# Optimization experiments

Hardware: AMD Instinct MI355X
Metric: run time of the kernel (lower is better)

The kernel has to match this reference:

```python
import jax, jax.numpy as jnp
import numpy as np

B, N, D_IN, D_MEM = 32, 1024, 512, 512
LN_EPS = 1e-5


def setup_inputs() -> dict:
    key = jax.random.key(0)
    ks = jax.random.split(key, 6)
    adj = jax.random.uniform(ks[0], (B, N, N), dtype=jnp.float32)
    input_emb = jax.random.normal(ks[1], (B * N, D_IN), dtype=jnp.float32)
    seq_lens = jnp.full((B,), N, dtype=jnp.int64) if jax.config.jax_enable_x64 else jnp.full((B,), N, dtype=jnp.int32)
    scale = 1.0 / np.sqrt(D_IN)
    W0_w = jax.random.normal(ks[2], (D_MEM, D_IN), dtype=jnp.float32) * scale
    W0_b = jax.random.normal(ks[3], (D_MEM,), dtype=jnp.float32) * 0.01
    W1_w = jax.random.normal(ks[4], (D_MEM, D_MEM), dtype=jnp.float32) * scale
    W1_b = jax.random.normal(ks[5], (D_MEM,), dtype=jnp.float32) * 0.01
    ln_g = jnp.ones((D_MEM,), dtype=jnp.float32)
    ln_b = jnp.zeros((D_MEM,), dtype=jnp.float32)
    return {"adj": adj, "input_emb": input_emb, "seq_lens": seq_lens,
            "W0_w": W0_w, "W0_b": W0_b, "W1_w": W1_w, "W1_b": W1_b,
            "ln_g": ln_g, "ln_b": ln_b}


def _layer_norm(x, g, b):
    mu = jnp.mean(x, axis=-1, keepdims=True)
    var = jnp.mean(jnp.square(x - mu), axis=-1, keepdims=True)
    return (x - mu) * jax.lax.rsqrt(var + LN_EPS) * g + b


def reference(adj, input_emb, seq_lens, W0_w, W0_b, W1_w, W1_b, ln_g, ln_b):
    # All seq_lens == N, so pad_sequence(split(input_emb)) is a pure reshape.
    x = input_emb.reshape(B, N, D_IN)  # dropout probs are 0 -> identity
    denom = jnp.sum(adj, axis=2, keepdims=True) + 1.0           # [B,N,1]
    masks = ((jnp.sum(adj, axis=2) + jnp.sum(adj, axis=1)) == 0)[..., None]  # [B,N,1]
    for Ww, Wb in ((W0_w, W0_b), (W1_w, W1_b)):
        Ax = jnp.einsum('bnm,bmd->bnd', adj, x)                 # adj.bmm(x)
        # W(Ax) + W(x) == (Ax + x) @ W^T + 2b
        AxW = (Ax + x) @ Ww.T + 2.0 * Wb
        x = jax.nn.relu(AxW / denom)                            # gcn_drop p=0
    out = _layer_norm(x, ln_g, ln_b)                            # norm_flag=True
    return out, masks
```

## Files before the change

### kernel.cpp

```cpp
#include <hip/hip_runtime.h>
#include <stdint.h>

typedef __bf16 bf16_t;
typedef __bf16 bf16x8 __attribute__((ext_vector_type(8)));
typedef float  f32x4  __attribute__((ext_vector_type(4)));

#define GLD_LDS(gp, lp) __builtin_amdgcn_global_load_lds( \
    (const __attribute__((address_space(1))) void*)(gp),  \
    (__attribute__((address_space(3))) void*)(lp), 16, 0, 0)

__global__ void probe_kernel(const unsigned int* __restrict__ w, int* __restrict__ flag)
{
    const int lane = threadIdx.x;
    bool ok = true;
#pragma unroll
    for (int i = 0; i < 4; ++i) {
        unsigned x = w[lane * 4 + i];
        unsigned lo = x & 0xffffu, hi = x >> 16;
        ok = ok && (lo <= 0x3F80u) && (hi <= 0x3F80u);
    }
    unsigned long long m = __ballot(ok);
    if (lane == 0) *flag = (m == ~0ULL) ? 1 : 0;
}

__device__ __forceinline__ void gemm_mainloop(const bf16_t* __restrict__ Ag,
                                              const bf16_t* __restrict__ Bg,
                                              int K, bf16_t* Abuf, bf16_t* Bbuf,
                                              f32x4 acc[4][4])
{
    const int t    = threadIdx.x;
    const int wave = t >> 6;
    const int lane = t & 63;
    const int srow = (wave << 5) + (lane >> 3);
    const int sc   = ((lane & 7) ^ (lane >> 3)) << 3;
    const bf16_t* aP = Ag + (size_t)srow * K + sc;
    const bf16_t* bP = Bg + (size_t)srow * K + sc;
    const size_t rskip = (size_t)8 * K;
    bf16_t* aL = Abuf + (wave << 11);
    bf16_t* bL = Bbuf + (wave << 11);
    const int wm   = (wave & 1) << 6;
    const int wn   = (wave >> 1) << 6;
    const int lrow = lane & 15;
    const int quad = lane >> 4;
    const int g    = lrow & 7;
    const int so[2] = { (quad ^ g) << 3, ((4 | quad) ^ g) << 3 };

#pragma unroll
    for (int i = 0; i < 4; ++i)
#pragma unroll
        for (int j = 0; j < 4; ++j)
#pragma unroll
            for (int r = 0; r < 4; ++r) acc[i][j][r] = 0.0f;

    for (int kk = 0; kk < K; kk += 64) {
#pragma unroll
        for (int p = 0; p < 4; ++p) {
            GLD_LDS(aP + p * rskip, aL + (p << 9));
            GLD_LDS(bP + p * rskip, bL + (p << 9));
        }
        aP += 64; bP += 64;
        __syncthreads();

#pragma unroll
        for (int s = 0; s < 2; ++s) {
            bf16x8 af[4], bfv[4];
#pragma unroll
            for (int i = 0; i < 4; ++i) {
                af[i]  = *(const bf16x8*)(Abuf + ((wm + (i << 4) + lrow) << 6) + so[s]);
                bfv[i] = *(const bf16x8*)(Bbuf + ((wn + (i << 4) + lrow) << 6) + so[s]);
            }
#pragma unroll
            for (int i = 0; i < 4; ++i)
#pragma unroll
                for (int j = 0; j < 4; ++j)
                    acc[i][j] = __builtin_amdgcn_mfma_f32_16x16x32_bf16(af[i], bfv[j], acc[i][j], 0, 0, 0);
        }
        __syncthreads();
    }
}

__global__ __launch_bounds__(256) void bmm_kernel(const void* __restrict__ adj_in,
                                                  const bf16_t* __restrict__ adj_ws,
                                                  const bf16_t* __restrict__ xT,
                                                  const void* __restrict__ xadd,
                                                  int xadd_bf16,
                                                  const int* __restrict__ flag,
                                                  bf16_t* __restrict__ zout)
{
    __shared__ __align__(16) bf16_t Abuf[8192];
    __shared__ __align__(16) bf16_t Bbuf[8192];
    const int is_bf = *flag;
    const bf16_t* adj = is_bf ? (const bf16_t*)adj_in : adj_ws;
    const int id   = blockIdx.x;
    const int xcd  = id & 7;
    const int slot = id >> 3;
    const int n0   = (slot & 3) << 7;
    const int m0   = ((slot >> 2) & 7) << 7;
    const int b    = (xcd << 2) | (slot >> 5);
    const bf16_t* Ag = adj + (size_t)b * 1048576 + (size_t)m0 * 1024;
    const bf16_t* Bg = xT  + (size_t)b * 524288  + (size_t)n0 * 1024;
    f32x4 acc[4][4];
    gemm_mainloop(Ag, Bg, 1024, Abuf, Bbuf, acc);

    const int lane = threadIdx.x & 63;
    const int wave = threadIdx.x >> 6;
    const int wm = (wave & 1) << 6, wn = (wave >> 1) << 6;
    const int lrow = lane & 15, quad = lane >> 4;
    const int xf32 = (!xadd_bf16) && (!is_bf);
    const size_t rowbase = (size_t)b * 1024 + m0;
#pragma unroll
    for (int i = 0; i < 4; ++i)
#pragma unroll
        for (int j = 0; j < 4; ++j)
#pragma unroll
            for (int r = 0; r < 4; ++r) {
                int row = wm + (i << 4) + (quad << 2) + r;
                int col = n0 + wn + (j << 4) + lrow;
                size_t idx = (rowbase + row) * 512 + col;
                float xa = xf32 ? ((const float*)xadd)[idx]
                                : (float)((const bf16_t*)xadd)[idx];
                zout[idx] = (bf16_t)(acc[i][j][r] + xa);
            }
}

__global__ __launch_bounds__(256) void wgemm_kernel(const bf16_t* __restrict__ z,
                                                    const bf16_t* __restrict__ W,
                                                    const float* __restrict__ bias,
                                                    const float* __restrict__ rowsum,
                                                    bf16_t* __restrict__ out)
{
    __shared__ __align__(16) bf16_t Abuf[8192];
    __shared__ __align__(16) bf16_t Bbuf[8192];
    const int m0 = blockIdx.x * 128;
    const int n0 = blockIdx.y * 128;
    const bf16_t* Ag = z + (size_t)m0 * 512;
    const bf16_t* Bg = W + (size_t)n0 * 512;
    f32x4 acc[4][4];
    gemm_mainloop(Ag, Bg, 512, Abuf, Bbuf, acc);

    const int lane = threadIdx.x & 63;
    const int wave = threadIdx.x >> 6;
    const int wm = (wave & 1) << 6, wn = (wave >> 1) << 6;
    const int lrow = lane & 15, quad = lane >> 4;
    float bi[4];
#pragma unroll
    for (int j = 0; j < 4; ++j) bi[j] = 2.0f * bias[n0 + wn + (j << 4) + lrow];
#pragma unroll
    for (int i = 0; i < 4; ++i)
#pragma unroll
        for (int r = 0; r < 4; ++r) {
            int row = m0 + wm + (i << 4) + (quad << 2) + r;
            float inv_dn = 1.0f / (rowsum[row] + 1.0f);
#pragma unroll
            for (int j = 0; j < 4; ++j) {
                int col = n0 + wn + (j << 4) + lrow;
                float v = fmaxf((acc[i][j][r] + bi[j]) * inv_dn, 0.0f);
                out[(size_t)row * 512 + col] = (bf16_t)v;
            }
        }
}

__global__ __launch_bounds__(256) void transpose_kernel(const void* __restrict__ in,
                                                        bf16_t* __restrict__ out,
                                                        const int* __restrict__ flag,
                                                        int force_bf16)
{
    __shared__ float tile[64][65];
    const int f32 = (!force_bf16) && (*flag == 0);
    const int b  = blockIdx.z;
    const int n0 = blockIdx.x * 64;
    const int d0 = blockIdx.y * 64;
    const int t  = threadIdx.x;
    const size_t base = ((size_t)b * 1024 + n0) * 512 + d0;
#pragma unroll
    for (int pass = 0; pass < 2; ++pass) {
        int r = pass * 32 + (t >> 3);
        int c = (t & 7) << 3;
        size_t off = base + (size_t)r * 512 + c;
        if (f32) {
            const float4* p = (const float4*)((const float*)in + off);
            float4 a = p[0], q = p[1];
            tile[r][c+0]=a.x; tile[r][c+1]=a.y; tile[r][c+2]=a.z; tile[r][c+3]=a.w;
            tile[r][c+4]=q.x; tile[r][c+5]=q.y; tile[r][c+6]=q.z; tile[r][c+7]=q.w;
        } else {
            bf16x8 v = *(const bf16x8*)((const bf16_t*)in + off);
#pragma unroll
            for (int k = 0; k < 8; ++k) tile[r][c + k] = (float)v[k];
        }
    }
    __syncthreads();
    bf16_t* dst = out + ((size_t)b * 512 + d0) * 1024 + n0;
#pragma unroll
    for (int pass = 0; pass < 2; ++pass) {
        int d = pass * 32 + (t >> 3);
        int c = (t & 7) << 3;
        bf16x8 v;
#pragma unroll
        for (int k = 0; k < 8; ++k) v[k] = (bf16_t)tile[c + k][d];
        *(bf16x8*)(dst + (size_t)d * 1024 + c) = v;
    }
}

__global__ __launch_bounds__(256) void adjrow_kernel(const void* __restrict__ adj,
                                                     const int* __restrict__ flag,
                                                     bf16_t* __restrict__ adj_b,
                                                     float* __restrict__ rowsum)
{
    const int row  = blockIdx.x * 4 + (threadIdx.x >> 6);
    const int lane = threadIdx.x & 63;
    const int f32  = (*flag == 0);
    const size_t base = (size_t)row * 1024 + lane * 16;
    float v[16];
    if (f32) {
        const float4* p = (const float4*)((const float*)adj + base);
#pragma unroll
        for (int i = 0; i < 4; ++i) {
            float4 q = p[i];
            v[i*4+0]=q.x; v[i*4+1]=q.y; v[i*4+2]=q.z; v[i*4+3]=q.w;
        }
    } else {
        const bf16x8* p = (const bf16x8*)((const bf16_t*)adj + base);
        bf16x8 q0 = p[0], q1 = p[1];
#pragma unroll
        for (int k = 0; k < 8; ++k) { v[k] = (float)q0[k]; v[8+k] = (float)q1[k]; }
    }
    float s = 0.0f;
#pragma unroll
    for (int k = 0; k < 16; ++k) s += v[k];
    if (f32) {
        bf16x8 o0, o1;
#pragma unroll
        for (int k = 0; k < 8; ++k) { o0[k] = (bf16_t)v[k]; o1[k] = (bf16_t)v[8+k]; }
        *(bf16x8*)(adj_b + base)     = o0;
        *(bf16x8*)(adj_b + base + 8) = o1;
    }
#pragma unroll
    for (int off = 32; off > 0; off >>= 1) s += __shfl_down(s, off);
    if (lane == 0) rowsum[row] = s;
}

__global__ __launch_bounds__(256) void colsum_kernel(const void* __restrict__ adj_in,
                                                     const bf16_t* __restrict__ adj_ws,
                                                     const int* __restrict__ flag,
                                                     float* __restrict__ colsum)
{
    const bf16_t* a = (*flag) ? (const bf16_t*)adj_in : adj_ws;
    const int b = blockIdx.y;
    const int c = blockIdx.x * 256 + threadIdx.x;
    const int r0 = blockIdx.z * 256;
    const bf16_t* p = a + (size_t)b * 1048576 + (size_t)r0 * 1024 + c;
    float s = 0.0f;
#pragma unroll 8
    for (int r = 0; r < 256; ++r) s += (float)p[(size_t)r * 1024];
    atomicAdd(&colsum[b * 1024 + c], s);
}

__global__ __launch_bounds__(256) void mask_kernel(const float* __restrict__ rowsum,
                                                   const float* __restrict__ colsum,
                                                   void* __restrict__ out,
                                                   const int* __restrict__ flag)
{
    const int i = blockIdx.x * 256 + threadIdx.x;
    float m = (rowsum[i] + colsum[i] == 0.0f) ? 1.0f : 0.0f;
    if (*flag) ((bf16_t*)out)[16777216 + i] = (bf16_t)m;
    else       ((float*)out)[16777216 + i]  = m;
}

__global__ __launch_bounds__(256) void canon_small(const void* __restrict__ W0,
                                                   const void* __restrict__ W1,
                                                   const void* __restrict__ b0,
                                                   const void* __restrict__ b1,
                                                   const void* __restrict__ g,
                                                   const void* __restrict__ bt,
                                                   const int* __restrict__ flag,
                                                   bf16_t* __restrict__ W0ws,
                                                   bf16_t* __restrict__ W1ws,
                                                   float* __restrict__ par,
                                                   float* __restrict__ colsum)
{
    const int idx = blockIdx.x * 256 + threadIdx.x;
    const int f32 = (*flag == 0);
#define RD(p, i) (f32 ? ((const float*)(p))[i] : (float)((const bf16_t*)(p))[i])
    if      (idx < 262144) W0ws[idx]          = (bf16_t)RD(W0, idx);
    else if (idx < 524288) W1ws[idx - 262144] = (bf16_t)RD(W1, idx - 262144);
    else if (idx < 524800) par[idx - 524288]  = RD(b0, idx - 524288);
    else if (idx < 525312) par[idx - 524288]  = RD(b1, idx - 524800);
    else if (idx < 525824) par[idx - 524288]  = RD(g,  idx - 525312);
    else if (idx < 526336) par[idx - 524288]  = RD(bt, idx - 525824);
    else if (idx < 559104) colsum[idx - 526336] = 0.0f;
#undef RD
}

__global__ __launch_bounds__(256) void ln_kernel(const bf16_t* __restrict__ x,
                                                 const float* __restrict__ g,
                                                 const float* __restrict__ bb,
                                                 void* __restrict__ out,
                                                 const int* __restrict__ flag)
{
    const int row  = blockIdx.x * 4 + (threadIdx.x >> 6);
    const int lane = threadIdx.x & 63;
    bf16x8 xv = *(const bf16x8*)(x + (size_t)row * 512 + lane * 8);
    float vv[8], s = 0.0f, ss = 0.0f;
#pragma unroll
    for (int k = 0; k < 8; ++k) { vv[k] = (float)xv[k]; s += vv[k]; ss += vv[k] * vv[k]; }
#pragma unroll
    for (int off = 32; off > 0; off >>= 1) { s += __shfl_down(s, off); ss += __shfl_down(ss, off); }
    s = __shfl(s, 0); ss = __shfl(ss, 0);
    const float mu   = s * (1.0f / 512.0f);
    const float var  = ss * (1.0f / 512.0f) - mu * mu;
    const float rstd = rsqrtf(var + 1e-5f);
    float o[8];
#pragma unroll
    for (int k = 0; k < 8; ++k)
        o[k] = (vv[k] - mu) * rstd * g[lane * 8 + k] + bb[lane * 8 + k];
    const size_t obase = (size_t)row * 512 + lane * 8;
    if (*flag) {
        bf16x8 ob;
#pragma unroll
        for (int k = 0; k < 8; ++k) ob[k] = (bf16_t)o[k];
        *(bf16x8*)((bf16_t*)out + obase) = ob;
    } else {
        float4 o0 = {o[0], o[1], o[2], o[3]}, o1 = {o[4], o[5], o[6], o[7]};
        *(float4*)((float*)out + obase)     = o0;
        *(float4*)((float*)out + obase + 4) = o1;
    }
}

extern "C" void kernel_launch(void* const* d_in, const int* in_sizes, int n_in,
                              void* d_out, int out_size, void* d_ws, size_t ws_size,
                              hipStream_t stream)
{
    const void* adj  = d_in[0];
    const void* x0   = d_in[1];
    const void* W0w  = d_in[3];
    const void* W0b  = d_in[4];
    const void* W1w  = d_in[5];
    const void* W1b  = d_in[6];
    const void* lng  = d_in[7];
    const void* lnb  = d_in[8];

    char* ws = (char*)d_ws;
    bf16_t* adj_ws = (bf16_t*)ws;
    bf16_t* x2     = (bf16_t*)ws;
    bf16_t* z_buf  = (bf16_t*)(ws + 67108864);
    bf16_t* x1     = (bf16_t*)(ws + 100663296);
    bf16_t* W0ws   = (bf16_t*)(ws + 134217728);
    bf16_t* W1ws   = (bf16_t*)(ws + 134742016);
    float*  par    = (float*)(ws + 135266304);
    float*  rowsum = (float*)(ws + 135274496);
    float*  colsum = (float*)(ws + 135405568);
    int*    flag   = (int*)(ws + 135536640);

    bf16_t* xT = (bf16_t*)d_out;

    probe_kernel<<<1, 64, 0, stream>>>((const unsigned int*)adj, flag);
    canon_small<<<2184, 256, 0, stream>>>(W0w, W1w, W0b, W1b, lng, lnb, flag,
                                          W0ws, W1ws, par, colsum);
    adjrow_kernel<<<8192, 256, 0, stream>>>(adj, flag, adj_ws, rowsum);
    colsum_kernel<<<dim3(4, 32, 4), 256, 0, stream>>>(adj, adj_ws, flag, colsum);
    mask_kernel<<<128, 256, 0, stream>>>(rowsum, colsum, d_out, flag);

    transpose_kernel<<<dim3(16, 8, 32), 256, 0, stream>>>(x0, xT, flag, 0);
    bmm_kernel<<<1024, 256, 0, stream>>>(adj, adj_ws, xT, x0, 0, flag, z_buf);
    wgemm_kernel<<<dim3(256, 4), 256, 0, stream>>>(z_buf, W0ws, par, rowsum, x1);

    transpose_kernel<<<dim3(16, 8, 32), 256, 0, stream>>>(x1, xT, flag, 1);
    bmm_kernel<<<1024, 256, 0, stream>>>(adj, adj_ws, xT, x1, 1, flag, z_buf);
    wgemm_kernel<<<dim3(256, 4), 256, 0, stream>>>(z_buf, W1ws, par + 512, rowsum, x2);

    ln_kernel<<<8192, 256, 0, stream>>>(x2, par + 1024, par + 1536, d_out, flag);
}
```

Measured before the change: 522.2 us.

## Rewrite GEMM mainloop as 256x256 tile with double-buffered 8-wave ping-pong pipeline

Replaces the 128x128 single-buffered GEMM mainloop, used by both the batched adjacency matmul and the weight GEMM, with a 256x256 tile on 512 threads. The new loop double-buffers A and B in 128KB of dynamic LDS and interleaves direct global-to-LDS loads with MFMA phases, using barriers, priority hints and vmcnt waits. The goal is to hide memory latency behind compute and double operand reuse per tile. In exchange the grids shrink to 256 blocks, which may under-fill the GPU, and register pressure rises with 32 accumulators per lane.

```diff
diff --git a/kernel.cpp b/kernel.cpp
--- a/kernel.cpp
+++ b/kernel.cpp
@@ -23,137 +23,192 @@
     if (lane == 0) *flag = (m == ~0ULL) ? 1 : 0;
 }
 
-__device__ __forceinline__ void gemm_mainloop(const bf16_t* __restrict__ Ag,
-                                              const bf16_t* __restrict__ Bg,
-                                              int K, bf16_t* Abuf, bf16_t* Bbuf,
-                                              f32x4 acc[4][4])
+#define STAGE_HALF(dstE, gp) do { \
+    GLD_LDS((gp) + (size_t)r0 * K + cS,        lds + (dstE) + t * 8); \
+    GLD_LDS((gp) + (size_t)(r0 + 64) * K + cS, lds + (dstE) + 4096 + t * 8); } while (0)
+
+#define STG_A(d, h, k0) STAGE_HALF((d)*16384 + (h)*8192, Ag + (size_t)(h)*128*K + (k0))
+#define STG_B(d, h, k0) STAGE_HALF(32768 + (d)*16384 + (h)*8192, Bg + (size_t)(h)*128*K + (k0))
+
+#define LDA(af, d, mq) do { _Pragma("unroll") for (int i_ = 0; i_ < 4; ++i_) { \
+    const bf16_t* p_ = lds + (d)*16384 + aBase + (((mq)*64) + (i_ << 4) + lrow) * 64; \
+    af[i_][0] = *(const bf16x8*)(p_ + so0); \
+    af[i_][1] = *(const bf16x8*)(p_ + so1); } } while (0)
+
+#define LDB(bfv, d, nq) do { _Pragma("unroll") for (int j_ = 0; j_ < 2; ++j_) { \
+    const bf16_t* p_ = lds + bBase + (d)*16384 + (((nq)*32) + (j_ << 4) + lrow) * 64; \
+    bfv[j_][0] = *(const bf16x8*)(p_ + so0); \
+    bfv[j_][1] = *(const bf16x8*)(p_ + so1); } } while (0)
+
+#define MFMA_Q(af, bfv, mq, nq) do { _Pragma("unroll") for (int i_ = 0; i_ < 4; ++i_) \
+    _Pragma("unroll") for (int j_ = 0; j_ < 2; ++j_) { \
+    acc[(mq)*4+i_][(nq)*2+j_] = __builtin_amdgcn_mfma_f32_16x16x32_bf16(af[i_][0], bfv[j_][0], acc[(mq)*4+i_][(nq)*2+j_], 0, 0, 0); \
+    acc[(mq)*4+i_][(nq)*2+j_] = __builtin_amdgcn_mfma_f32_16x16x32_bf16(af[i_][1], bfv[j_][1], acc[(mq)*4+i_][(nq)*2+j_], 0, 0, 0); } } while (0)
+
+#define PHASE_SYNC() do { __builtin_amdgcn_s_barrier(); \
+    asm volatile("s_waitcnt lgkmcnt(0)" ::: "memory"); \
+    __builtin_amdgcn_sched_barrier(0); \
+    __builtin_amdgcn_s_setprio(1); } while (0)
+
+#define PHASE_END() do { __builtin_amdgcn_s_setprio(0); \
+    __builtin_amdgcn_s_barrier(); } while (0)
+
+#define PHASE_END_VM() do { __builtin_amdgcn_s_setprio(0); \
+    asm volatile("s_waitcnt vmcnt(4)" ::: "memory"); \
+    __builtin_amdgcn_s_barrier(); } while (0)
+
+__device__ __forceinline__ void gemm256_mainloop(const bf16_t* __restrict__ Ag,
+                                                 const bf16_t* __restrict__ Bg,
+                                                 const int K, bf16_t* lds,
+                                                 f32x4 acc[8][4])
 {
     const int t    = threadIdx.x;
     const int wave = t >> 6;
     const int lane = t & 63;
-    const int srow = (wave << 5) + (lane >> 3);
-    const int sc   = ((lane & 7) ^ (lane >> 3)) << 3;
-    const bf16_t* aP = Ag + (size_t)srow * K + sc;
-    const bf16_t* bP = Bg + (size_t)srow * K + sc;
-    const size_t rskip = (size_t)8 * K;
-    bf16_t* aL = Abuf + (wave << 11);
-    bf16_t* bL = Bbuf + (wave << 11);
-    const int wm   = (wave & 1) << 6;
-    const int wn   = (wave >> 1) << 6;
+    const int wr   = wave >> 2;
+    const int wc   = wave & 3;
     const int lrow = lane & 15;
     const int quad = lane >> 4;
     const int g    = lrow & 7;
-    const int so[2] = { (quad ^ g) << 3, ((4 | quad) ^ g) << 3 };
-
-#pragma unroll
-    for (int i = 0; i < 4; ++i)
+
+    const int r0 = t >> 3;
+    const int cS = ((t & 7) ^ ((t >> 3) & 7)) << 3;
+
+    const int aBase = wr * 8192;
+    const int bBase = 32768 + ((wc >> 1) * 8192) + ((wc & 1) * 4096);
+    const int so0 = (quad ^ g) << 3;
+    const int so1 = ((4 | quad) ^ g) << 3;
+
+#pragma unroll
+    for (int i = 0; i < 8; ++i)
 #pragma unroll
         for (int j = 0; j < 4; ++j)
 #pragma unroll
             for (int r = 0; r < 4; ++r) acc[i][j][r] = 0.0f;
 
-    for (int kk = 0; kk < K; kk += 64) {
-#pragma unroll
-        for (int p = 0; p < 4; ++p) {
-            GLD_LDS(aP + p * rskip, aL + (p << 9));
-            GLD_LDS(bP + p * rskip, bL + (p << 9));
-        }
-        aP += 64; bP += 64;
-        __syncthreads();
-
-#pragma unroll
-        for (int s = 0; s < 2; ++s) {
-            bf16x8 af[4], bfv[4];
-#pragma unroll
-            for (int i = 0; i < 4; ++i) {
-                af[i]  = *(const bf16x8*)(Abuf + ((wm + (i << 4) + lrow) << 6) + so[s]);
-                bfv[i] = *(const bf16x8*)(Bbuf + ((wn + (i << 4) + lrow) << 6) + so[s]);
-            }
-#pragma unroll
-            for (int i = 0; i < 4; ++i)
-#pragma unroll
-                for (int j = 0; j < 4; ++j)
-                    acc[i][j] = __builtin_amdgcn_mfma_f32_16x16x32_bf16(af[i], bfv[j], acc[i][j], 0, 0, 0);
-        }
-        __syncthreads();
-    }
-}
-
-__global__ __launch_bounds__(256) void bmm_kernel(const void* __restrict__ adj_in,
-                                                  const bf16_t* __restrict__ adj_ws,
-                                                  const bf16_t* __restrict__ xT,
-                                                  const void* __restrict__ xadd,
-                                                  int xadd_bf16,
-                                                  const int* __restrict__ flag,
-                                                  bf16_t* __restrict__ zout)
-{
-    __shared__ __align__(16) bf16_t Abuf[8192];
-    __shared__ __align__(16) bf16_t Bbuf[8192];
+    STG_A(0, 0, 0); STG_A(0, 1, 0);
+    STG_B(0, 0, 0); STG_B(0, 1, 0);
+    STG_B(1, 0, 64); STG_B(1, 1, 64);
+    asm volatile("s_waitcnt vmcnt(4)" ::: "memory");
+    __builtin_amdgcn_s_barrier();
+
+    const int NT  = K >> 6;
+    const int NIT = NT >> 1;
+
+    bf16x8 af0[4][2], af1[4][2], ba[2][2], bb[2][2];
+
+    for (int it = 0; it < NIT; ++it) {
+        const int kA1 = (2 * it + 1) << 6;
+        const int k2  = ((2 * it + 2) < NT ? (2 * it + 2) : 0) << 6;
+        const int k3  = ((2 * it + 3) < NT ? (2 * it + 3) : 0) << 6;
+
+        LDA(af0, 0, 0); LDB(ba, 0, 0); STG_A(1, 0, kA1);
+        PHASE_SYNC(); MFMA_Q(af0, ba, 0, 0); PHASE_END();
+
+        LDB(bb, 0, 1); STG_A(1, 1, kA1);
+        PHASE_SYNC(); MFMA_Q(af0, bb, 0, 1); PHASE_END();
+
+        LDA(af1, 0, 1); STG_B(0, 0, k2);
+        PHASE_SYNC(); MFMA_Q(af1, ba, 1, 0); PHASE_END();
+
+        STG_B(0, 1, k2);
+        PHASE_SYNC(); MFMA_Q(af1, bb, 1, 1); PHASE_END_VM();
+
+        LDA(af0, 1, 0); LDB(ba, 1, 0); STG_A(0, 0, k2);
+        PHASE_SYNC(); MFMA_Q(af0, ba, 0, 0); PHASE_END();
+
+        LDB(bb, 1, 1); STG_A(0, 1, k2);
+        PHASE_SYNC(); MFMA_Q(af0, bb, 0, 1); PHASE_END();
+
+        LDA(af1, 1, 1); STG_B(1, 0, k3);
+        PHASE_SYNC(); MFMA_Q(af1, ba, 1, 0); PHASE_END();
+
+        STG_B(1, 1, k3);
+        PHASE_SYNC(); MFMA_Q(af1, bb, 1, 1); PHASE_END_VM();
+    }
+    asm volatile("s_waitcnt vmcnt(0)" ::: "memory");
+}
+
+__global__ __launch_bounds__(512, 2) void bmm_kernel(const void* __restrict__ adj_in,
+                                                     const bf16_t* __restrict__ adj_ws,
+                                                     const bf16_t* __restrict__ xT,
+                                                     const void* __restrict__ xadd,
+                                                     int xadd_bf16,
+                                                     const int* __restrict__ flag,
+                                                     bf16_t* __restrict__ zout)
+{
+    extern __shared__ __align__(16) bf16_t lds[];
     const int is_bf = *flag;
     const bf16_t* adj = is_bf ? (const bf16_t*)adj_in : adj_ws;
     const int id   = blockIdx.x;
     const int xcd  = id & 7;
-    const int slot = id >> 3;
-    const int n0   = (slot & 3) << 7;
-    const int m0   = ((slot >> 2) & 7) << 7;
-    const int b    = (xcd << 2) | (slot >> 5);
-    const bf16_t* Ag = adj + (size_t)b * 1048576 + (size_t)m0 * 1024;
-    const bf16_t* Bg = xT  + (size_t)b * 524288  + (size_t)n0 * 1024;
-    f32x4 acc[4][4];
-    gemm_mainloop(Ag, Bg, 1024, Abuf, Bbuf, acc);
+    const int s    = id >> 3;
+    const int b    = (xcd << 2) | (s >> 3);
+    const int tl   = s & 7;
+    const int mt   = tl >> 1;
+    const int nt2  = tl & 1;
+    const bf16_t* Ag = adj + (size_t)b * 1048576 + (size_t)mt * 262144;
+    const bf16_t* Bg = xT  + (size_t)b * 524288  + (size_t)nt2 * 262144;
+    f32x4 acc[8][4];
+    gemm256_mainloop(Ag, Bg, 1024, lds, acc);
 
     const int lane = threadIdx.x & 63;
     const int wave = threadIdx.x >> 6;
-    const int wm = (wave & 1) << 6, wn = (wave >> 1) << 6;
+    const int wr = wave >> 2, wc = wave & 3;
     const int lrow = lane & 15, quad = lane >> 4;
     const int xf32 = (!xadd_bf16) && (!is_bf);
-    const size_t rowbase = (size_t)b * 1024 + m0;
-#pragma unroll
-    for (int i = 0; i < 4; ++i)
+    const size_t rowbase = (size_t)b * 1024 + mt * 256 + wr * 128;
+    const int colbase = nt2 * 256 + wc * 64;
+#pragma unroll
+    for (int i = 0; i < 8; ++i)
 #pragma unroll
         for (int j = 0; j < 4; ++j)
 #pragma unroll
             for (int r = 0; r < 4; ++r) {
-                int row = wm + (i << 4) + (quad << 2) + r;
-                int col = n0 + wn + (j << 4) + lrow;
-                size_t idx = (rowbase + row) * 512 + col;
+                size_t row = rowbase + (i << 4) + (quad << 2) + r;
+                int col = colbase + (j << 4) + lrow;
+                size_t idx = row * 512 + col;
                 float xa = xf32 ? ((const float*)xadd)[idx]
                                 : (float)((const bf16_t*)xadd)[idx];
                 zout[idx] = (bf16_t)(acc[i][j][r] + xa);
             }
 }
 
-__global__ __launch_bounds__(256) void wgemm_kernel(const bf16_t* __restrict__ z,
-                                                    const bf16_t* __restrict__ W,
-                                                    const float* __restrict__ bias,
-                                                    const float* __restrict__ rowsum,
-                                                    bf16_t* __restrict__ out)
-{
-    __shared__ __align__(16) bf16_t Abuf[8192];
-    __shared__ __align__(16) bf16_t Bbuf[8192];
-    const int m0 = blockIdx.x * 128;
-    const int n0 = blockIdx.y * 128;
-    const bf16_t* Ag = z + (size_t)m0 * 512;
-    const bf16_t* Bg = W + (size_t)n0 * 512;
-    f32x4 acc[4][4];
-    gemm_mainloop(Ag, Bg, 512, Abuf, Bbuf, acc);
+__global__ __launch_bounds__(512, 2) void wgemm_kernel(const bf16_t* __restrict__ z,
+                                                       const bf16_t* __restrict__ W,
+                                                       const float* __restrict__ bias,
+                                                       const float* __restrict__ rowsum,
+                                                       bf16_t* __restrict__ out)
+{
+    extern __shared__ __align__(16) bf16_t lds[];
+    const int id  = blockIdx.x;
+    const int xcd = id & 7;
+    const int s   = id >> 3;
+    const int mt  = (xcd << 4) | (s >> 1);
+    const int nt2 = s & 1;
+    const bf16_t* Ag = z + (size_t)mt * 131072;
+    const bf16_t* Bg = W + (size_t)nt2 * 131072;
+    f32x4 acc[8][4];
+    gemm256_mainloop(Ag, Bg, 512, lds, acc);
 
     const int lane = threadIdx.x & 63;
     const int wave = threadIdx.x >> 6;
-    const int wm = (wave & 1) << 6, wn = (wave >> 1) << 6;
+    const int wr = wave >> 2, wc = wave & 3;
     const int lrow = lane & 15, quad = lane >> 4;
+    const int m0 = mt * 256 + wr * 128;
+    const int n0 = nt2 * 256 + wc * 64;
     float bi[4];
 #pragma unroll
-    for (int j = 0; j < 4; ++j) bi[j] = 2.0f * bias[n0 + wn + (j << 4) + lrow];
-#pragma unroll
-    for (int i = 0; i < 4; ++i)
+    for (int j = 0; j < 4; ++j) bi[j] = 2.0f * bias[n0 + (j << 4) + lrow];
+#pragma unroll
+    for (int i = 0; i < 8; ++i)
 #pragma unroll
         for (int r = 0; r < 4; ++r) {
-            int row = m0 + wm + (i << 4) + (quad << 2) + r;
+            int row = m0 + (i << 4) + (quad << 2) + r;
             float inv_dn = 1.0f / (rowsum[row] + 1.0f);
 #pragma unroll
             for (int j = 0; j < 4; ++j) {
-                int col = n0 + wn + (j << 4) + lrow;
+                int col = n0 + (j << 4) + lrow;
                 float v = fmaxf((acc[i][j][r] + bi[j]) * inv_dn, 0.0f);
                 out[(size_t)row * 512 + col] = (bf16_t)v;
             }
@@ -353,6 +408,11 @@
 
     bf16_t* xT = (bf16_t*)d_out;
 
+    hipFuncSetAttribute((const void*)bmm_kernel,
+                        hipFuncAttributeMaxDynamicSharedMemorySize, 131072);
+    hipFuncSetAttribute((const void*)wgemm_kernel,
+                        hipFuncAttributeMaxDynamicSharedMemorySize, 131072);
+
     probe_kernel<<<1, 64, 0, stream>>>((const unsigned int*)adj, flag);
     canon_small<<<2184, 256, 0, stream>>>(W0w, W1w, W0b, W1b, lng, lnb, flag,
                                           W0ws, W1ws, par, colsum);
@@ -361,12 +421,12 @@
     mask_kernel<<<128, 256, 0, stream>>>(rowsum, colsum, d_out, flag);
 
     transpose_kernel<<<dim3(16, 8, 32), 256, 0, stream>>>(x0, xT, flag, 0);
-    bmm_kernel<<<1024, 256, 0, stream>>>(adj, adj_ws, xT, x0, 0, flag, z_buf);
-    wgemm_kernel<<<dim3(256, 4), 256, 0, stream>>>(z_buf, W0ws, par, rowsum, x1);
+    bmm_kernel<<<256, 512, 131072, stream>>>(adj, adj_ws, xT, x0, 0, flag, z_buf);
+    wgemm_kernel<<<256, 512, 131072, stream>>>(z_buf, W0ws, par, rowsum, x1);
 
     transpose_kernel<<<dim3(16, 8, 32), 256, 0, stream>>>(x1, xT, flag, 1);
-    bmm_kernel<<<1024, 256, 0, stream>>>(adj, adj_ws, xT, x1, 1, flag, z_buf);
-    wgemm_kernel<<<dim3(256, 4), 256, 0, stream>>>(z_buf, W1ws, par + 512, rowsum, x2);
+    bmm_kernel<<<256, 512, 131072, stream>>>(adj, adj_ws, xT, x1, 1, flag, z_buf);
+    wgemm_kernel<<<256, 512, 131072, stream>>>(z_buf, W1ws, par + 512, rowsum, x2);
 
     ln_kernel<<<8192, 256, 0, stream>>>(x2, par + 1024, par + 1536, d_out, flag);
 }
```

Measured after the change: 492.9 us. 1.06x faster.
